# Kernel optimization log

Measured on AMD Instinct MI355X. Metric: run time of the kernel, lower is better.

The kernel has to match this reference:

```python
import jax, jax.numpy as jnp
import numpy as np

DIM = 16      # sdefunc.dim (latent channels)
S = 64        # spatial side of latent volume
HID = 64      # drift conv hidden channels
DT = 0.05     # sdeint dt
SIGMA = 0.1   # diagonal diffusion coefficient
N_STEPS = 20  # (t1 - t0) / dt with ts = [0, 1]


def conv3d(v, w, b):
    # v: [B, C, D, H, W], w: [O, I, 3, 3, 3]
    y = jax.lax.conv_general_dilated(
        v, w, window_strides=(1, 1, 1), padding='SAME',
        dimension_numbers=('NCDHW', 'OIDHW', 'NCDHW'))
    return y + b[None, :, None, None, None]


def setup_inputs() -> dict:
    key = jax.random.key(0)
    k = jax.random.split(key, 6)
    x = jax.random.normal(k[0], (1, DIM, S, S, S), dtype=jnp.float32)
    integration_time = jnp.arange(2, dtype=jnp.float32)  # ts = [0.0, 1.0]
    # drift network params (Conv3d(DIM->HID) -> tanh -> Conv3d(HID->DIM))
    w1 = jax.random.normal(k[1], (HID, DIM, 3, 3, 3), dtype=jnp.float32) / np.sqrt(DIM * 27)
    b1 = jnp.zeros((HID,), dtype=jnp.float32)
    w2 = jax.random.normal(k[2], (DIM, HID, 3, 3, 3), dtype=jnp.float32) / np.sqrt(HID * 27)
    b2 = jnp.zeros((DIM,), dtype=jnp.float32)
    # pre-sampled standard-normal Brownian increments, one per Euler step
    noise = jax.random.normal(k[3], (N_STEPS, 1, DIM * S * S * S), dtype=jnp.float32)
    return {"x": x, "integration_time": integration_time,
            "w1": w1, "b1": b1, "w2": w2, "b2": b2, "noise": noise}


def reference(x, integration_time, w1, b1, w2, b2, noise):
    B = x.shape[0]  # == 1 (required by the original reshape)
    y0 = x.reshape(B, -1)  # [B, DIM*S^3]
    sqrt_dt = jnp.float32(DT ** 0.5)

    def drift(y):
        v = y.reshape(B, DIM, S, S, S)
        h = jnp.tanh(conv3d(v, w1, b1))
        f = conv3d(h, w2, b2)
        return f.reshape(B, -1)

    def step(y, z):
        # Euler-Maruyama, diagonal noise: y += f(t,y) dt + sigma * sqrt(dt) * z
        y = y + drift(y) * DT + SIGMA * sqrt_dt * z
        return y, None

    yT, _ = jax.lax.scan(step, y0, noise)
    out = yT.reshape(DIM, S, S, S)  # out[-1] of the trajectory (B == 1)
    return out[None]  # [1, DIM, S, S, S]
```

## Files before the change

### kernel.cpp

```cpp
#include <hip/hip_runtime.h>


#define S    64
#define SS   4096
#define SSS  262144
#define DT_F 0.05f
#define SIG_SDT 0.022360679774997897f
#define PD   66

typedef __bf16 bf16x8 __attribute__((ext_vector_type(8)));
typedef float  f32x4  __attribute__((ext_vector_type(4)));
typedef float  f32x16 __attribute__((ext_vector_type(16)));

union B8U { uint4 u; bf16x8 b; };
__device__ inline bf16x8 as_bf16x8(uint4 u) { B8U x; x.u = u; return x.b; }

__device__ inline unsigned short bf16_bits(float f) {
    union { float f; unsigned u; } c; c.f = f;
    unsigned r = c.u + 0x7fffu + ((c.u >> 16) & 1u);
    return (unsigned short)(r >> 16);
}

__device__ inline float tanh_fast(float v) {
    float a = fminf(fmaxf(v, -15.f), 15.f);
    float e = __expf(2.f * a);
    return (e - 1.f) * __builtin_amdgcn_rcpf(e + 1.f);
}

__global__ void zero_ws(uint4* __restrict__ p, unsigned n)
{
    const uint4 z = {0u, 0u, 0u, 0u};
    for (unsigned i = blockIdx.x * 256u + threadIdx.x; i < n; i += gridDim.x * 256u)
        p[i] = z;
}

__global__ void prep_weights(const float* __restrict__ w1, const float* __restrict__ w2,
                             unsigned short* __restrict__ w1t, unsigned short* __restrict__ w2t)
{
    const int t = blockIdx.x * 256 + threadIdx.x;
    if (t >= 27 * 2 * 64 * 8) return;
    const int j = t & 7, l = (t >> 3) & 63, half = (t >> 9) & 1, tap = t >> 10;
    {
        const int oc = half * 32 + (l & 31), ic = (l >> 5) * 8 + j;
        w1t[t] = bf16_bits(w1[(oc * 16 + ic) * 27 + tap]);
    }
    {
        const int oc = l & 15, ic = half * 32 + (l >> 4) * 8 + j;
        w2t[t] = bf16_bits(w2[(oc * 64 + ic) * 27 + tap]);
    }
}

__global__ void pack_x(const float* __restrict__ x, char* __restrict__ ybp)
{
    const int p = blockIdx.x * 256 + threadIdx.x;
    const int z = p >> 12, yy = (p >> 6) & 63, xx = p & 63;
    union { unsigned short s[16]; uint4 v[2]; } pk;
    #pragma unroll
    for (int c = 0; c < 16; ++c) pk.s[c] = bf16_bits(x[c * SSS + p]);
    char* dst = ybp + (((size_t)(z + 1) * PD + (yy + 1)) * PD + (xx + 1)) * 32;
    *(uint4*)dst        = pk.v[0];
    *(uint4*)(dst + 16) = pk.v[1];
}

__global__ __launch_bounds__(256, 2)
void conv1_mfma(const char* __restrict__ ybp, const uint4* __restrict__ w1t,
                const float* __restrict__ b1, char* __restrict__ hbp)
{
    const int t = threadIdx.x, lane = t & 63, w = t >> 6;
    const int mt = w >> 1, xg = w & 1;
    const int y = blockIdx.y, z0 = blockIdx.x * 8;
    const int n = lane & 31, hh = lane >> 5;
    const int x0 = xg * 32;

    bf16x8 A[27];
    #pragma unroll
    for (int tap = 0; tap < 27; ++tap)
        A[tap] = as_bf16x8(w1t[(tap * 2 + mt) * 64 + lane]);

    float bias[16];
    #pragma unroll
    for (int q = 0; q < 4; ++q)
        #pragma unroll
        for (int j = 0; j < 4; ++j)
            bias[q * 4 + j] = b1[mt * 32 + q * 8 + hh * 4 + j];

    const char* ybl = ybp + (x0 + n) * 32 + hh * 16;
    char* hbl = hbp + ((size_t)(y + 1) * PD + (x0 + n + 1)) * 128
                    + (mt * 32 + hh * 4) * 2;

    f32x16 acc[3];
    #pragma unroll
    for (int s = 0; s < 3; ++s)
        #pragma unroll
        for (int q = 0; q < 16; ++q) acc[s][q] = 0.f;

    #pragma unroll
    for (int i = 0; i < 10; ++i) {
        const int zp = z0 - 1 + i;
        const char* pb = ybl + ((size_t)(zp + 1) * PD + y) * (PD * 32);
        #pragma unroll
        for (int dy = 0; dy < 3; ++dy) {
            #pragma unroll
            for (int dx = 0; dx < 3; ++dx) {
                bf16x8 B = as_bf16x8(*(const uint4*)(pb + (dy * PD + dx) * 32));
                if (i < 8)
                    acc[(i + 1) % 3] = __builtin_amdgcn_mfma_f32_32x32x16_bf16(
                        A[0 + dy * 3 + dx], B, acc[(i + 1) % 3], 0, 0, 0);
                if (i >= 1 && i <= 8)
                    acc[i % 3] = __builtin_amdgcn_mfma_f32_32x32x16_bf16(
                        A[9 + dy * 3 + dx], B, acc[i % 3], 0, 0, 0);
                if (i >= 2)
                    acc[(i + 2) % 3] = __builtin_amdgcn_mfma_f32_32x32x16_bf16(
                        A[18 + dy * 3 + dx], B, acc[(i + 2) % 3], 0, 0, 0);
            }
        }
        if (i >= 2) {
            const int z = zp - 1;
            char* hp = hbl + (size_t)(z + 1) * (PD * PD * 128);
            f32x16 a = acc[(i + 2) % 3];
            #pragma unroll
            for (int q = 0; q < 4; ++q) {
                union { unsigned short sh[4]; uint2 v; } pk;
                #pragma unroll
                for (int j = 0; j < 4; ++j)
                    pk.sh[j] = bf16_bits(tanh_fast(a[q * 4 + j] + bias[q * 4 + j]));
                *(uint2*)(hp + q * 16) = pk.v;
            }
            #pragma unroll
            for (int q = 0; q < 16; ++q) acc[(i + 2) % 3][q] = 0.f;
        }
    }
}

__global__ __launch_bounds__(128, 3)
void conv2_mfma(const char* __restrict__ hbp, const uint4* __restrict__ w2t,
                const float* __restrict__ b2, const float* __restrict__ ysrc,
                float* __restrict__ ydst, char* __restrict__ ybp,
                const float* __restrict__ nz)
{
    __shared__ f32x4 scratch[2][64];
    const int t = threadIdx.x, lane = t & 63, kc = t >> 6;
    const int y = blockIdx.y, z0 = blockIdx.z * 8, x0 = blockIdx.x * 16;
    const int n16 = lane & 15, g = lane >> 4;

    bf16x8 A[27];
    #pragma unroll
    for (int tap = 0; tap < 27; ++tap)
        A[tap] = as_bf16x8(w2t[(tap * 2 + kc) * 64 + lane]);

    float b2v[4];
    #pragma unroll
    for (int j = 0; j < 4; ++j) b2v[j] = b2[g * 4 + j];

    const char* hbl = hbp + (x0 + n16) * 128 + kc * 64 + g * 16;

    f32x4 acc[3];
    #pragma unroll
    for (int s = 0; s < 3; ++s)
        #pragma unroll
        for (int q = 0; q < 4; ++q) acc[s][q] = 0.f;

    #pragma unroll
    for (int i = 0; i < 10; ++i) {
        const int zp = z0 - 1 + i;
        const char* pb = hbl + ((size_t)(zp + 1) * PD + y) * (PD * 128);
        #pragma unroll
        for (int dy = 0; dy < 3; ++dy) {
            #pragma unroll
            for (int dx = 0; dx < 3; ++dx) {
                bf16x8 B = as_bf16x8(*(const uint4*)(pb + (dy * PD + dx) * 128));
                if (i < 8)
                    acc[(i + 1) % 3] = __builtin_amdgcn_mfma_f32_16x16x32_bf16(
                        A[0 + dy * 3 + dx], B, acc[(i + 1) % 3], 0, 0, 0);
                if (i >= 1 && i <= 8)
                    acc[i % 3] = __builtin_amdgcn_mfma_f32_16x16x32_bf16(
                        A[9 + dy * 3 + dx], B, acc[i % 3], 0, 0, 0);
                if (i >= 2)
                    acc[(i + 2) % 3] = __builtin_amdgcn_mfma_f32_16x16x32_bf16(
                        A[18 + dy * 3 + dx], B, acc[(i + 2) % 3], 0, 0, 0);
            }
        }
        if (i >= 2) {
            const int z = zp - 1;
            f32x4 a = acc[(i + 2) % 3];
            #pragma unroll
            for (int q = 0; q < 4; ++q) acc[(i + 2) % 3][q] = 0.f;
            if (kc == 1) scratch[i & 1][lane] = a;
            __syncthreads();
            if (kc == 0) {
                f32x4 o = scratch[i & 1][lane];
                const size_t p = (size_t)z * SS + y * S + (x0 + n16);
                union { unsigned short sh[4]; uint2 v; } pk;
                #pragma unroll
                for (int j = 0; j < 4; ++j) {
                    const size_t idx = (size_t)(g * 4 + j) * SSS + p;
                    const float f  = a[j] + o[j] + b2v[j];
                    const float yv = ysrc[idx] + f * DT_F + SIG_SDT * nz[idx];
                    ydst[idx] = yv;
                    pk.sh[j] = bf16_bits(yv);
                }
                char* yb = ybp + (((size_t)(z + 1) * PD + (y + 1)) * PD
                                  + (x0 + n16 + 1)) * 32 + g * 8;
                *(uint2*)yb = pk.v;
            }
        }
    }
}

extern "C" void kernel_launch(void* const* d_in, const int* in_sizes, int n_in,
                              void* d_out, int out_size, void* d_ws, size_t ws_size,
                              hipStream_t stream)
{
    (void)in_sizes; (void)n_in; (void)out_size; (void)ws_size;
    const float* x     = (const float*)d_in[0];
    const float* w1    = (const float*)d_in[2];
    const float* b1    = (const float*)d_in[3];
    const float* w2    = (const float*)d_in[4];
    const float* b2    = (const float*)d_in[5];
    const float* noise = (const float*)d_in[6];

    char* ws = (char*)d_ws;
    unsigned short* w1t = (unsigned short*)ws;
    unsigned short* w2t = (unsigned short*)(ws + 55296);
    char* ybp = ws + 131072;
    char* hbp = ws + 131072 + 9199872;
    float* y  = (float*)d_out;

    zero_ws<<<2048, 256, 0, stream>>>((uint4*)ybp, (9199872u + 36799488u) / 16u);
    prep_weights<<<108, 256, 0, stream>>>(w1, w2, w1t, w2t);
    pack_x<<<1024, 256, 0, stream>>>(x, ybp);

    for (int s = 0; s < 20; ++s) {
        conv1_mfma<<<dim3(8, 64), 256, 0, stream>>>(
            ybp, (const uint4*)w1t, b1, hbp);
        const float* ys = (s == 0) ? x : (const float*)y;
        conv2_mfma<<<dim3(4, 64, 8), 128, 0, stream>>>(
            hbp, (const uint4*)w2t, b2, ys, y, ybp,
            noise + (size_t)s * (16 * SSS));
    }
}
```

Baseline: 2.141 ms.

## Fuse all Euler steps into one persistent kernel with grid-wide barriers

```diff
diff --git a/kernel.cpp b/kernel.cpp
--- a/kernel.cpp
+++ b/kernel.cpp
@@ -7,6 +7,7 @@
 #define DT_F 0.05f
 #define SIG_SDT 0.022360679774997897f
 #define PD   66
+#define NBLK 256
 
 typedef __bf16 bf16x8 __attribute__((ext_vector_type(8)));
 typedef float  f32x4  __attribute__((ext_vector_type(4)));
@@ -22,9 +23,8 @@
 }
 
 __device__ inline float tanh_fast(float v) {
-    float a = fminf(fmaxf(v, -15.f), 15.f);
-    float e = __expf(2.f * a);
-    return (e - 1.f) * __builtin_amdgcn_rcpf(e + 1.f);
+    float e = __expf(2.f * v);
+    return 1.f - 2.f * __builtin_amdgcn_rcpf(e + 1.f);
 }
 
 __global__ void zero_ws(uint4* __restrict__ p, unsigned n)
@@ -35,9 +35,11 @@
 }
 
 __global__ void prep_weights(const float* __restrict__ w1, const float* __restrict__ w2,
-                             unsigned short* __restrict__ w1t, unsigned short* __restrict__ w2t)
+                             unsigned short* __restrict__ w1t, unsigned short* __restrict__ w2t,
+                             unsigned* __restrict__ bar)
 {
     const int t = blockIdx.x * 256 + threadIdx.x;
+    if (blockIdx.x == 0 && threadIdx.x < 64) bar[threadIdx.x] = 0u;
     if (t >= 27 * 2 * 64 * 8) return;
     const int j = t & 7, l = (t >> 3) & 63, half = (t >> 9) & 1, tap = t >> 10;
     {
@@ -62,148 +64,183 @@
     *(uint4*)(dst + 16) = pk.v[1];
 }
 
-__global__ __launch_bounds__(256, 2)
-void conv1_mfma(const char* __restrict__ ybp, const uint4* __restrict__ w1t,
-                const float* __restrict__ b1, char* __restrict__ hbp)
-{
+__device__ inline void gbar(unsigned* cnt, unsigned* gen)
+{
+    __syncthreads();
+    if (threadIdx.x == 0) {
+        __threadfence();
+        unsigned g0 = __hip_atomic_load(gen, __ATOMIC_RELAXED, __HIP_MEMORY_SCOPE_AGENT);
+        unsigned a  = __hip_atomic_fetch_add(cnt, 1u, __ATOMIC_ACQ_REL, __HIP_MEMORY_SCOPE_AGENT);
+        if (a == NBLK - 1u) {
+            __hip_atomic_store(cnt, 0u, __ATOMIC_RELAXED, __HIP_MEMORY_SCOPE_AGENT);
+            __hip_atomic_fetch_add(gen, 1u, __ATOMIC_RELEASE, __HIP_MEMORY_SCOPE_AGENT);
+        } else {
+            unsigned gg;
+            do {
+                __builtin_amdgcn_s_sleep(8);
+                gg = __hip_atomic_load(gen, __ATOMIC_ACQUIRE, __HIP_MEMORY_SCOPE_AGENT);
+            } while (gg == g0);
+        }
+        __threadfence();
+    }
+    __syncthreads();
+}
+
+__global__ __launch_bounds__(512, 2)
+void sde_mega(const uint4* __restrict__ w1t, const uint4* __restrict__ w2t,
+              const float* __restrict__ b1, const float* __restrict__ b2,
+              const float* __restrict__ x, float* __restrict__ yst,
+              char* __restrict__ ybp, char* __restrict__ hbp,
+              const float* __restrict__ noise, unsigned* bar)
+{
+    __shared__ f32x4 scratch[2][2][2][64];
     const int t = threadIdx.x, lane = t & 63, w = t >> 6;
-    const int mt = w >> 1, xg = w & 1;
-    const int y = blockIdx.y, z0 = blockIdx.x * 8;
-    const int n = lane & 31, hh = lane >> 5;
-    const int x0 = xg * 32;
-
-    bf16x8 A[27];
-    #pragma unroll
-    for (int tap = 0; tap < 27; ++tap)
-        A[tap] = as_bf16x8(w1t[(tap * 2 + mt) * 64 + lane]);
-
-    float bias[16];
-    #pragma unroll
-    for (int q = 0; q < 4; ++q)
-        #pragma unroll
-        for (int j = 0; j < 4; ++j)
-            bias[q * 4 + j] = b1[mt * 32 + q * 8 + hh * 4 + j];
-
-    const char* ybl = ybp + (x0 + n) * 32 + hh * 16;
-    char* hbl = hbp + ((size_t)(y + 1) * PD + (x0 + n + 1)) * 128
-                    + (mt * 32 + hh * 4) * 2;
-
-    f32x16 acc[3];
-    #pragma unroll
-    for (int s = 0; s < 3; ++s)
-        #pragma unroll
-        for (int q = 0; q < 16; ++q) acc[s][q] = 0.f;
-
-    #pragma unroll
-    for (int i = 0; i < 10; ++i) {
-        const int zp = z0 - 1 + i;
-        const char* pb = ybl + ((size_t)(zp + 1) * PD + y) * (PD * 32);
-        #pragma unroll
-        for (int dy = 0; dy < 3; ++dy) {
-            #pragma unroll
-            for (int dx = 0; dx < 3; ++dx) {
-                bf16x8 B = as_bf16x8(*(const uint4*)(pb + (dy * PD + dx) * 32));
-                if (i < 8)
-                    acc[(i + 1) % 3] = __builtin_amdgcn_mfma_f32_32x32x16_bf16(
-                        A[0 + dy * 3 + dx], B, acc[(i + 1) % 3], 0, 0, 0);
-                if (i >= 1 && i <= 8)
-                    acc[i % 3] = __builtin_amdgcn_mfma_f32_32x32x16_bf16(
-                        A[9 + dy * 3 + dx], B, acc[i % 3], 0, 0, 0);
-                if (i >= 2)
-                    acc[(i + 2) % 3] = __builtin_amdgcn_mfma_f32_32x32x16_bf16(
-                        A[18 + dy * 3 + dx], B, acc[(i + 2) % 3], 0, 0, 0);
+    const int bs = ((int)blockIdx.x & 7) * 32 + ((int)blockIdx.x >> 3);
+    const int yy = bs & 63, bz = bs >> 6;
+
+    const int n   = lane & 31, hh = lane >> 5;
+    const int n16 = lane & 15, g  = lane >> 4;
+    const int zs  = w >> 2;
+    const int mt  = (w >> 1) & 1, xg1 = w & 1;
+    const int xh2 = (w >> 1) & 1, kc  = w & 1;
+    const int z0  = bz * 16 + zs * 8;
+
+    unsigned* cnt = bar;
+    unsigned* gen = bar + 32;
+
+    #pragma unroll 1
+    for (int s = 0; s < 20; ++s) {
+        {
+            asm volatile("" ::: "memory");
+            bf16x8 A[27];
+            #pragma unroll
+            for (int tap = 0; tap < 27; ++tap)
+                A[tap] = as_bf16x8(w1t[(tap * 2 + mt) * 64 + lane]);
+            float bias[16];
+            #pragma unroll
+            for (int q = 0; q < 4; ++q)
+                #pragma unroll
+                for (int j = 0; j < 4; ++j)
+                    bias[q * 4 + j] = b1[mt * 32 + q * 8 + hh * 4 + j];
+
+            const char* ybl = ybp + (xg1 * 32 + n) * 32 + hh * 16;
+            char* hbl = hbp + ((size_t)(yy + 1) * PD + (xg1 * 32 + n + 1)) * 128
+                            + (mt * 32 + hh * 4) * 2;
+
+            f32x16 acc[3];
+            #pragma unroll
+            for (int r = 0; r < 3; ++r)
+                #pragma unroll
+                for (int q = 0; q < 16; ++q) acc[r][q] = 0.f;
+
+            #pragma unroll
+            for (int i = 0; i < 10; ++i) {
+                const int zp = z0 - 1 + i;
+                const char* pb = ybl + ((size_t)(zp + 1) * PD + yy) * (PD * 32);
+                #pragma unroll
+                for (int dy = 0; dy < 3; ++dy)
+                    #pragma unroll
+                    for (int dx = 0; dx < 3; ++dx) {
+                        bf16x8 B = as_bf16x8(*(const uint4*)(pb + (dy * PD + dx) * 32));
+                        if (i < 8)
+                            acc[(i + 1) % 3] = __builtin_amdgcn_mfma_f32_32x32x16_bf16(
+                                A[0 + dy * 3 + dx], B, acc[(i + 1) % 3], 0, 0, 0);
+                        if (i >= 1 && i <= 8)
+                            acc[i % 3] = __builtin_amdgcn_mfma_f32_32x32x16_bf16(
+                                A[9 + dy * 3 + dx], B, acc[i % 3], 0, 0, 0);
+                        if (i >= 2)
+                            acc[(i + 2) % 3] = __builtin_amdgcn_mfma_f32_32x32x16_bf16(
+                                A[18 + dy * 3 + dx], B, acc[(i + 2) % 3], 0, 0, 0);
+                    }
+                if (i >= 2) {
+                    const int z = z0 + i - 2;
+                    char* hp = hbl + (size_t)(z + 1) * (PD * PD * 128);
+                    f32x16 a = acc[(i + 2) % 3];
+                    #pragma unroll
+                    for (int q = 0; q < 4; ++q) {
+                        union { unsigned short sh[4]; uint2 v; } pk;
+                        #pragma unroll
+                        for (int j = 0; j < 4; ++j)
+                            pk.sh[j] = bf16_bits(tanh_fast(a[q * 4 + j] + bias[q * 4 + j]));
+                        *(uint2*)(hp + q * 16) = pk.v;
+                    }
+                    #pragma unroll
+                    for (int q = 0; q < 16; ++q) acc[(i + 2) % 3][q] = 0.f;
+                }
             }
         }
-        if (i >= 2) {
-            const int z = zp - 1;
-            char* hp = hbl + (size_t)(z + 1) * (PD * PD * 128);
-            f32x16 a = acc[(i + 2) % 3];
-            #pragma unroll
-            for (int q = 0; q < 4; ++q) {
-                union { unsigned short sh[4]; uint2 v; } pk;
-                #pragma unroll
-                for (int j = 0; j < 4; ++j)
-                    pk.sh[j] = bf16_bits(tanh_fast(a[q * 4 + j] + bias[q * 4 + j]));
-                *(uint2*)(hp + q * 16) = pk.v;
-            }
-            #pragma unroll
-            for (int q = 0; q < 16; ++q) acc[(i + 2) % 3][q] = 0.f;
-        }
-    }
-}
-
-__global__ __launch_bounds__(128, 3)
-void conv2_mfma(const char* __restrict__ hbp, const uint4* __restrict__ w2t,
-                const float* __restrict__ b2, const float* __restrict__ ysrc,
-                float* __restrict__ ydst, char* __restrict__ ybp,
-                const float* __restrict__ nz)
-{
-    __shared__ f32x4 scratch[2][64];
-    const int t = threadIdx.x, lane = t & 63, kc = t >> 6;
-    const int y = blockIdx.y, z0 = blockIdx.z * 8, x0 = blockIdx.x * 16;
-    const int n16 = lane & 15, g = lane >> 4;
-
-    bf16x8 A[27];
-    #pragma unroll
-    for (int tap = 0; tap < 27; ++tap)
-        A[tap] = as_bf16x8(w2t[(tap * 2 + kc) * 64 + lane]);
-
-    float b2v[4];
-    #pragma unroll
-    for (int j = 0; j < 4; ++j) b2v[j] = b2[g * 4 + j];
-
-    const char* hbl = hbp + (x0 + n16) * 128 + kc * 64 + g * 16;
-
-    f32x4 acc[3];
-    #pragma unroll
-    for (int s = 0; s < 3; ++s)
-        #pragma unroll
-        for (int q = 0; q < 4; ++q) acc[s][q] = 0.f;
-
-    #pragma unroll
-    for (int i = 0; i < 10; ++i) {
-        const int zp = z0 - 1 + i;
-        const char* pb = hbl + ((size_t)(zp + 1) * PD + y) * (PD * 128);
-        #pragma unroll
-        for (int dy = 0; dy < 3; ++dy) {
-            #pragma unroll
-            for (int dx = 0; dx < 3; ++dx) {
-                bf16x8 B = as_bf16x8(*(const uint4*)(pb + (dy * PD + dx) * 128));
-                if (i < 8)
-                    acc[(i + 1) % 3] = __builtin_amdgcn_mfma_f32_16x16x32_bf16(
-                        A[0 + dy * 3 + dx], B, acc[(i + 1) % 3], 0, 0, 0);
-                if (i >= 1 && i <= 8)
-                    acc[i % 3] = __builtin_amdgcn_mfma_f32_16x16x32_bf16(
-                        A[9 + dy * 3 + dx], B, acc[i % 3], 0, 0, 0);
-                if (i >= 2)
-                    acc[(i + 2) % 3] = __builtin_amdgcn_mfma_f32_16x16x32_bf16(
-                        A[18 + dy * 3 + dx], B, acc[(i + 2) % 3], 0, 0, 0);
+        gbar(cnt, gen);
+        {
+            asm volatile("" ::: "memory");
+            bf16x8 A[27];
+            #pragma unroll
+            for (int tap = 0; tap < 27; ++tap)
+                A[tap] = as_bf16x8(w2t[(tap * 2 + kc) * 64 + lane]);
+            float b2v[4];
+            #pragma unroll
+            for (int j = 0; j < 4; ++j) b2v[j] = b2[g * 4 + j];
+
+            const float* ysrc = (s == 0) ? x : yst;
+            const float* nz = noise + (size_t)s * (16 * SSS);
+
+            #pragma unroll 1
+            for (int xt = 0; xt < 2; ++xt) {
+                const int x0 = xh2 * 32 + xt * 16;
+                const char* hbl = hbp + (x0 + n16) * 128 + kc * 64 + g * 16;
+
+                f32x4 acc[3];
+                #pragma unroll
+                for (int r = 0; r < 3; ++r)
+                    #pragma unroll
+                    for (int q = 0; q < 4; ++q) acc[r][q] = 0.f;
+
+                #pragma unroll
+                for (int i = 0; i < 10; ++i) {
+                    const int zp = z0 - 1 + i;
+                    const char* pb = hbl + ((size_t)(zp + 1) * PD + yy) * (PD * 128);
+                    #pragma unroll
+                    for (int dy = 0; dy < 3; ++dy)
+                        #pragma unroll
+                        for (int dx = 0; dx < 3; ++dx) {
+                            bf16x8 B = as_bf16x8(*(const uint4*)(pb + (dy * PD + dx) * 128));
+                            if (i < 8)
+                                acc[(i + 1) % 3] = __builtin_amdgcn_mfma_f32_16x16x32_bf16(
+                                    A[0 + dy * 3 + dx], B, acc[(i + 1) % 3], 0, 0, 0);
+                            if (i >= 1 && i <= 8)
+                                acc[i % 3] = __builtin_amdgcn_mfma_f32_16x16x32_bf16(
+                                    A[9 + dy * 3 + dx], B, acc[i % 3], 0, 0, 0);
+                            if (i >= 2)
+                                acc[(i + 2) % 3] = __builtin_amdgcn_mfma_f32_16x16x32_bf16(
+                                    A[18 + dy * 3 + dx], B, acc[(i + 2) % 3], 0, 0, 0);
+                        }
+                    if (i >= 2) {
+                        const int z = z0 + i - 2;
+                        f32x4 a = acc[(i + 2) % 3];
+                        #pragma unroll
+                        for (int q = 0; q < 4; ++q) acc[(i + 2) % 3][q] = 0.f;
+                        if (kc == 1) scratch[zs][xh2][i & 1][lane] = a;
+                        __syncthreads();
+                        if (kc == 0) {
+                            f32x4 o = scratch[zs][xh2][i & 1][lane];
+                            const size_t p = (size_t)z * SS + yy * S + (x0 + n16);
+                            union { unsigned short sh[4]; uint2 v; } pk;
+                            #pragma unroll
+                            for (int j = 0; j < 4; ++j) {
+                                const size_t idx = (size_t)(g * 4 + j) * SSS + p;
+                                const float f = a[j] + o[j] + b2v[j];
+                                const float yv = ysrc[idx] + f * DT_F + SIG_SDT * nz[idx];
+                                yst[idx] = yv;
+                                pk.sh[j] = bf16_bits(yv);
+                            }
+                            char* yb = ybp + (((size_t)(z + 1) * PD + (yy + 1)) * PD
+                                              + (x0 + n16 + 1)) * 32 + g * 8;
+                            *(uint2*)yb = pk.v;
+                        }
+                    }
+                }
             }
         }
-        if (i >= 2) {
-            const int z = zp - 1;
-            f32x4 a = acc[(i + 2) % 3];
-            #pragma unroll
-            for (int q = 0; q < 4; ++q) acc[(i + 2) % 3][q] = 0.f;
-            if (kc == 1) scratch[i & 1][lane] = a;
-            __syncthreads();
-            if (kc == 0) {
-                f32x4 o = scratch[i & 1][lane];
-                const size_t p = (size_t)z * SS + y * S + (x0 + n16);
-                union { unsigned short sh[4]; uint2 v; } pk;
-                #pragma unroll
-                for (int j = 0; j < 4; ++j) {
-                    const size_t idx = (size_t)(g * 4 + j) * SSS + p;
-                    const float f  = a[j] + o[j] + b2v[j];
-                    const float yv = ysrc[idx] + f * DT_F + SIG_SDT * nz[idx];
-                    ydst[idx] = yv;
-                    pk.sh[j] = bf16_bits(yv);
-                }
-                char* yb = ybp + (((size_t)(z + 1) * PD + (y + 1)) * PD
-                                  + (x0 + n16 + 1)) * 32 + g * 8;
-                *(uint2*)yb = pk.v;
-            }
-        }
+        gbar(cnt, gen);
     }
 }
 
@@ -222,20 +259,15 @@
     char* ws = (char*)d_ws;
     unsigned short* w1t = (unsigned short*)ws;
     unsigned short* w2t = (unsigned short*)(ws + 55296);
+    unsigned* bar = (unsigned*)(ws + 110592);
     char* ybp = ws + 131072;
     char* hbp = ws + 131072 + 9199872;
     float* y  = (float*)d_out;
 
     zero_ws<<<2048, 256, 0, stream>>>((uint4*)ybp, (9199872u + 36799488u) / 16u);
-    prep_weights<<<108, 256, 0, stream>>>(w1, w2, w1t, w2t);
+    prep_weights<<<108, 256, 0, stream>>>(w1, w2, w1t, w2t, bar);
     pack_x<<<1024, 256, 0, stream>>>(x, ybp);
 
-    for (int s = 0; s < 20; ++s) {
-        conv1_mfma<<<dim3(8, 64), 256, 0, stream>>>(
-            ybp, (const uint4*)w1t, b1, hbp);
-        const float* ys = (s == 0) ? x : (const float*)y;
-        conv2_mfma<<<dim3(4, 64, 8), 128, 0, stream>>>(
-            hbp, (const uint4*)w2t, b2, ys, y, ybp,
-            noise + (size_t)s * (16 * SSS));
-    }
-}
+    sde_mega<<<dim3(NBLK), dim3(512), 0, stream>>>(
+        (const uint4*)w1t, (const uint4*)w2t, b1, b2, x, y, ybp, hbp, noise, bar);
+}
```

Result: slower. 4.662 ms (+117.7%).
